# Kernel optimization log

Hardware: AMD Instinct MI355X
Metric: run time of the kernel (lower is better)

## Reference

```python
import jax, jax.numpy as jnp
import numpy as np

N = 100000      # nodes
E = 1600000     # nonzeros in sparse H (avg degree 16)
IN_DIM = 128
HID = 128
OUT = 128


def setup_inputs() -> dict:
    key = jax.random.key(0)
    k = jax.random.split(key, 8)
    X = jax.random.normal(k[0], (N, IN_DIM), dtype=jnp.float32)
    H_rows = jax.random.randint(k[1], (E,), 0, N, dtype=jnp.int32)
    H_cols = jax.random.randint(k[2], (E,), 0, N, dtype=jnp.int32)
    H_vals = jax.random.uniform(k[3], (E,), dtype=jnp.float32)
    # Linear params (PyTorch: y = x @ W.T + b); store as [in, out] for x @ W
    s1 = 1.0 / np.sqrt(IN_DIM)
    s2 = 1.0 / np.sqrt(HID)
    W1 = jax.random.uniform(k[4], (IN_DIM, HID), jnp.float32, -s1, s1)
    b1 = jax.random.uniform(k[5], (HID,), jnp.float32, -s1, s1)
    W2 = jax.random.uniform(k[6], (HID, OUT), jnp.float32, -s2, s2)
    b2 = jax.random.uniform(k[7], (OUT,), jnp.float32, -s2, s2)
    return {"X": X, "H_rows": H_rows, "H_cols": H_cols, "H_vals": H_vals,
            "W1": W1, "b1": b1, "W2": W2, "b2": b2}


def _spmm(rows, cols, vals, X):
    # sparse [N,N] @ dense [N,d] via edge gather + segment-sum
    msgs = vals[:, None] * X[cols]            # [E, d]
    return jax.ops.segment_sum(msgs, rows, num_segments=N)


def reference(X, H_rows, H_cols, H_vals, W1, b1, W2, b2):
    # num_layers == 2 branch; dropout is identity (eval mode)
    h = _spmm(H_rows, H_cols, H_vals, X @ W1 + b1)   # H @ W1(X)
    h = jax.nn.relu(h)
    out = _spmm(H_rows, H_cols, H_vals, h @ W2 + b2) # H @ W2(h)
    return out
```

## Files before the change

### kernel.cpp

```cpp
#include <hip/hip_runtime.h>

#define NNODES 100000
#define DIM 128
#define BROWS 256
#define NB ((NNODES + BROWS - 1) / BROWS)
#define BCAP 5120
#define CHUNK 4096

__device__ __forceinline__ float f4c(const float4& v, int q) {
    switch (q) { case 0: return v.x; case 1: return v.y; case 2: return v.z; }
    return v.w;
}

__device__ __forceinline__ unsigned int pack_bf16x2(float lo, float hi) {
    unsigned int ul = __float_as_uint(lo);
    unsigned int uh = __float_as_uint(hi);
    ul = (ul + 0x7fffu + ((ul >> 16) & 1u)) >> 16;
    uh = (uh + 0x7fffu + ((uh >> 16) & 1u)) & 0xffff0000u;
    return uh | ul;
}

__device__ __forceinline__ void unpack_bf16x8(uint4 v, float* f) {
    f[0] = __uint_as_float(v.x << 16); f[1] = __uint_as_float(v.x & 0xffff0000u);
    f[2] = __uint_as_float(v.y << 16); f[3] = __uint_as_float(v.y & 0xffff0000u);
    f[4] = __uint_as_float(v.z << 16); f[5] = __uint_as_float(v.z & 0xffff0000u);
    f[6] = __uint_as_float(v.w << 16); f[7] = __uint_as_float(v.w & 0xffff0000u);
}

template <bool IN_BF16>
__global__ __launch_bounds__(256, 2) void gemm_tile(const void* __restrict__ Ain,
                                                    const float* __restrict__ W,
                                                    const float* __restrict__ bias,
                                                    unsigned short* __restrict__ Yb, int n) {
    __shared__ float as[128 * 36];
    __shared__ float bs[32 * 128];
    const int t = threadIdx.x;
    const int tx = t & 15, ty = t >> 4;
    const int row0 = blockIdx.x * 128;
    const int r_lo = ty * 4;
    const int c_lo = tx * 4;

    float acc[8][8];
    {
        const float4 bv0 = *(const float4*)&bias[c_lo];
        const float4 bv1 = *(const float4*)&bias[64 + c_lo];
#pragma unroll
        for (int i = 0; i < 8; ++i) {
            acc[i][0] = bv0.x; acc[i][1] = bv0.y; acc[i][2] = bv0.z; acc[i][3] = bv0.w;
            acc[i][4] = bv1.x; acc[i][5] = bv1.y; acc[i][6] = bv1.z; acc[i][7] = bv1.w;
        }
    }

    const float4* W4 = (const float4*)W;

    for (int kp = 0; kp < 4; ++kp) {
        if (IN_BF16) {
            const uint4* A16 = (const uint4*)Ain;
#pragma unroll
            for (int j = 0; j < 2; ++j) {
                const int l = t + j * 256;
                const int row = l >> 2, ch = l & 3;
                const int rr = row0 + row;
                uint4 v = make_uint4(0u, 0u, 0u, 0u);
                if (rr < n) v = A16[(size_t)rr * 16 + kp * 4 + ch];
                float f[8];
                unpack_bf16x8(v, f);
                float* dst = &as[row * 36 + ch * 8];
                *(float4*)&dst[0] = make_float4(f[0], f[1], f[2], f[3]);
                *(float4*)&dst[4] = make_float4(f[4], f[5], f[6], f[7]);
            }
        } else {
            const float4* A4 = (const float4*)Ain;
#pragma unroll
            for (int j = 0; j < 4; ++j) {
                const int l = t + j * 256;
                const int row = l >> 3, k4 = l & 7;
                const int rr = row0 + row;
                float4 v = make_float4(0.f, 0.f, 0.f, 0.f);
                if (rr < n) v = A4[(size_t)rr * 32 + kp * 8 + k4];
                *(float4*)&as[row * 36 + k4 * 4] = v;
            }
        }
#pragma unroll
        for (int j = 0; j < 4; ++j) {
            const int l = t + j * 256;
            const int k = l >> 5, c4 = l & 31;
            *(float4*)&bs[k * 128 + c4 * 4] = W4[(size_t)(kp * 32 + k) * 32 + c4];
        }
        __syncthreads();

#pragma unroll 2
        for (int kk = 0; kk < 32; kk += 4) {
            float4 a[8], b0[4], b1[4];
#pragma unroll
            for (int i = 0; i < 4; ++i) {
                a[i]     = *(const float4*)&as[(r_lo + i) * 36 + kk];
                a[4 + i] = *(const float4*)&as[(64 + r_lo + i) * 36 + kk];
            }
#pragma unroll
            for (int q = 0; q < 4; ++q) {
                b0[q] = *(const float4*)&bs[(kk + q) * 128 + c_lo];
                b1[q] = *(const float4*)&bs[(kk + q) * 128 + 64 + c_lo];
            }
#pragma unroll
            for (int q = 0; q < 4; ++q) {
#pragma unroll
                for (int i = 0; i < 8; ++i) {
                    const float av = f4c(a[i], q);
                    acc[i][0] = fmaf(av, b0[q].x, acc[i][0]);
                    acc[i][1] = fmaf(av, b0[q].y, acc[i][1]);
                    acc[i][2] = fmaf(av, b0[q].z, acc[i][2]);
                    acc[i][3] = fmaf(av, b0[q].w, acc[i][3]);
                    acc[i][4] = fmaf(av, b1[q].x, acc[i][4]);
                    acc[i][5] = fmaf(av, b1[q].y, acc[i][5]);
                    acc[i][6] = fmaf(av, b1[q].z, acc[i][6]);
                    acc[i][7] = fmaf(av, b1[q].w, acc[i][7]);
                }
            }
        }
        __syncthreads();
    }

#pragma unroll
    for (int i = 0; i < 8; ++i) {
        const int lr = (i < 4) ? (r_lo + i) : (64 + r_lo + i - 4);
        const int rr = row0 + lr;
        if (rr < n) {
            uint2 lo = make_uint2(pack_bf16x2(acc[i][0], acc[i][1]),
                                  pack_bf16x2(acc[i][2], acc[i][3]));
            uint2 hi = make_uint2(pack_bf16x2(acc[i][4], acc[i][5]),
                                  pack_bf16x2(acc[i][6], acc[i][7]));
            *(uint2*)&Yb[(size_t)rr * DIM + c_lo] = lo;
            *(uint2*)&Yb[(size_t)rr * DIM + 64 + c_lo] = hi;
        }
    }
}

__global__ __launch_bounds__(256) void pass1_bin(const int* __restrict__ rows,
                                                 const int* __restrict__ cols,
                                                 const float* __restrict__ vals,
                                                 int* __restrict__ bcnt,
                                                 int2* __restrict__ tmp, int nnz) {
    __shared__ int hist[NB];
    __shared__ int base[NB];
    __shared__ int cur[NB];
    const int t = threadIdx.x;
    const int e0 = blockIdx.x * CHUNK;
    const int e1 = min(e0 + CHUNK, nnz);

    for (int i = t; i < NB; i += 256) { hist[i] = 0; cur[i] = 0; }
    __syncthreads();

    for (int i = e0 + t; i < e1; i += 256)
        atomicAdd(&hist[rows[i] >> 8], 1);
    __syncthreads();

    for (int i = t; i < NB; i += 256)
        base[i] = (hist[i] > 0) ? atomicAdd(&bcnt[i], hist[i]) : 0;
    __syncthreads();

    for (int i = e0 + t; i < e1; i += 256) {
        const int r = rows[i];
        const int b = r >> 8;
        const int pos = base[b] + atomicAdd(&cur[b], 1);
        if (pos < BCAP)
            tmp[(size_t)b * BCAP + pos] =
                make_int2(((r & 255) << 24) | cols[i], __float_as_int(vals[i]));
    }
}

__global__ __launch_bounds__(512) void scan_buckets(const int* __restrict__ bcnt,
                                                    int* __restrict__ bbase, int nb) {
    __shared__ int s[512];
    const int t = threadIdx.x;
    const int v = (t < nb) ? bcnt[t] : 0;
    s[t] = v;
    __syncthreads();
    for (int off = 1; off < 512; off <<= 1) {
        int x = (t >= off) ? s[t - off] : 0;
        __syncthreads();
        s[t] += x;
        __syncthreads();
    }
    if (t < nb) bbase[t] = s[t] - v;
}

__global__ __launch_bounds__(256) void pass2_sort(const int2* __restrict__ tmp,
                                                  const int* __restrict__ bcnt,
                                                  const int* __restrict__ bbase,
                                                  int2* __restrict__ epack,
                                                  int* __restrict__ row_ptr,
                                                  int* __restrict__ counts, int n) {
    __shared__ int cnt[256];
    __shared__ int s[256];
    __shared__ int cur[256];
    const int b = blockIdx.x;
    const int t = threadIdx.x;
    const int row0 = b * BROWS;
    const int nrows = min(BROWS, n - row0);
    const int m = min(bcnt[b], BCAP);
    const int base = bbase[b];
    const int2* __restrict__ src = tmp + (size_t)b * BCAP;

    cnt[t] = 0;
    __syncthreads();
    for (int i = t; i < m; i += 256)
        atomicAdd(&cnt[((unsigned)src[i].x) >> 24], 1);
    __syncthreads();

    const int v = cnt[t];
    s[t] = v;
    __syncthreads();
    for (int off = 1; off < 256; off <<= 1) {
        int x = (t >= off) ? s[t - off] : 0;
        __syncthreads();
        s[t] += x;
        __syncthreads();
    }
    const int excl = s[t] - v;
    if (t < nrows) {
        row_ptr[row0 + t] = base + excl;
        counts[row0 + t] = v;
    }
    cur[t] = base + excl;
    __syncthreads();

    for (int i = t; i < m; i += 256) {
        const int2 e = src[i];
        const int rl = ((unsigned)e.x) >> 24;
        const int pos = atomicAdd(&cur[rl], 1);
        epack[pos] = make_int2(e.x & 0xFFFFFF, e.y);
    }
}

template <bool RELU_OUT, bool OUT_BF16>
__global__ __launch_bounds__(256) void spmm_csr(const int* __restrict__ row_ptr,
                                                const int* __restrict__ counts,
                                                const int2* __restrict__ epack,
                                                const unsigned short* __restrict__ Xb,
                                                void* __restrict__ out, int n) {
    const int gid = blockIdx.x * blockDim.x + threadIdx.x;
    const int r = gid >> 4;
    const int lane = gid & 15;
    if (r >= n) return;
    const int start = row_ptr[r];
    const int cnt = counts[r];
    const uint4* __restrict__ X16 = (const uint4*)Xb;
    const int2* __restrict__ ep = epack + start;

    float acc[8];
#pragma unroll
    for (int k = 0; k < 8; ++k) acc[k] = 0.f;

    int j = 0;
    for (; j + 4 <= cnt; j += 4) {
        const int2 e0 = ep[j], e1 = ep[j + 1], e2 = ep[j + 2], e3 = ep[j + 3];
        const uint4 x0 = X16[(size_t)e0.x * 16 + lane];
        const uint4 x1 = X16[(size_t)e1.x * 16 + lane];
        const uint4 x2 = X16[(size_t)e2.x * 16 + lane];
        const uint4 x3 = X16[(size_t)e3.x * 16 + lane];
        const float v0 = __int_as_float(e0.y), v1 = __int_as_float(e1.y);
        const float v2 = __int_as_float(e2.y), v3 = __int_as_float(e3.y);
        float f0[8], f1[8], f2[8], f3[8];
        unpack_bf16x8(x0, f0); unpack_bf16x8(x1, f1);
        unpack_bf16x8(x2, f2); unpack_bf16x8(x3, f3);
#pragma unroll
        for (int k = 0; k < 8; ++k)
            acc[k] += v0 * f0[k] + v1 * f1[k] + v2 * f2[k] + v3 * f3[k];
    }
    for (; j < cnt; ++j) {
        const int2 e = ep[j];
        const uint4 x = X16[(size_t)e.x * 16 + lane];
        const float v = __int_as_float(e.y);
        float f[8];
        unpack_bf16x8(x, f);
#pragma unroll
        for (int k = 0; k < 8; ++k) acc[k] += v * f[k];
    }

    if (RELU_OUT) {
#pragma unroll
        for (int k = 0; k < 8; ++k) acc[k] = fmaxf(acc[k], 0.f);
    }

    if (OUT_BF16) {
        uint4 pv = make_uint4(pack_bf16x2(acc[0], acc[1]), pack_bf16x2(acc[2], acc[3]),
                              pack_bf16x2(acc[4], acc[5]), pack_bf16x2(acc[6], acc[7]));
        ((uint4*)out)[(size_t)r * 16 + lane] = pv;
    } else {
        float* of = (float*)out;
        *(float4*)&of[(size_t)r * DIM + lane * 8]     = make_float4(acc[0], acc[1], acc[2], acc[3]);
        *(float4*)&of[(size_t)r * DIM + lane * 8 + 4] = make_float4(acc[4], acc[5], acc[6], acc[7]);
    }
}

extern "C" void kernel_launch(void* const* d_in, const int* in_sizes, int n_in,
                              void* d_out, int out_size, void* d_ws, size_t ws_size,
                              hipStream_t stream) {
    const float* X      = (const float*)d_in[0];
    const int*   H_rows = (const int*)d_in[1];
    const int*   H_cols = (const int*)d_in[2];
    const float* H_vals = (const float*)d_in[3];
    const float* W1     = (const float*)d_in[4];
    const float* b1     = (const float*)d_in[5];
    const float* W2     = (const float*)d_in[6];
    const float* b2     = (const float*)d_in[7];
    float* out = (float*)d_out;

    const int E = in_sizes[1];
    const int N = NNODES;
    const size_t bmat_bytes = (size_t)N * DIM * 2;

    const int gemm_blocks = (N + 127) / 128;
    const int p1_blocks = (E + CHUNK - 1) / CHUNK;
    const int spmm_blocks = (N * 16 + 255) / 256;

    char* p = (char*)d_ws;
    unsigned short* Yb = (unsigned short*)p;  p += bmat_bytes;
    unsigned short* hb = (unsigned short*)p;  p += bmat_bytes;
    int2* epack        = (int2*)p;            p += (size_t)E * 8;
    int2* tmp          = (int2*)p;            p += (size_t)NB * BCAP * 8;
    int*  bcnt         = (int*)p;             p += (size_t)NB * 4;
    int*  bbase        = (int*)p;             p += (size_t)NB * 4;
    int*  row_ptr      = (int*)p;             p += (size_t)N * 4;
    int*  counts       = (int*)p;             p += (size_t)N * 4;

    hipMemsetAsync(bcnt, 0, (size_t)NB * 4, stream);
    pass1_bin<<<p1_blocks, 256, 0, stream>>>(H_rows, H_cols, H_vals, bcnt, tmp, E);
    scan_buckets<<<1, 512, 0, stream>>>(bcnt, bbase, NB);
    pass2_sort<<<NB, 256, 0, stream>>>(tmp, bcnt, bbase, epack, row_ptr, counts, N);

    gemm_tile<false><<<gemm_blocks, 256, 0, stream>>>(X, W1, b1, Yb, N);
    spmm_csr<true, true><<<spmm_blocks, 256, 0, stream>>>(row_ptr, counts, epack, Yb, hb, N);

    gemm_tile<true><<<gemm_blocks, 256, 0, stream>>>(hb, W2, b2, Yb, N);
    spmm_csr<false, false><<<spmm_blocks, 256, 0, stream>>>(row_ptr, counts, epack, Yb, out, N);
}
```

Baseline: 397.6 us.

## Replace FP32 SIMT GEMM with FP16 MFMA GEMM using pre-transposed weights

Swaps the shared-memory tiled FP32 FMA GEMM for a register-only kernel built on 16x16x32 f16 MFMA instructions. Each wave loads its 32 input rows straight from global memory into half8 fragments. A new prep kernel transposes and converts W1/W2 to FP16 so weight fragments load contiguously. This targets the dense-layer compute cost but lowers input and weight precision to FP16. Weight fragments are also reloaded from global memory per block rather than staged in LDS.

Result: faster. 364.1 us (-8.4%).

```diff
diff --git a/kernel.cpp b/kernel.cpp
--- a/kernel.cpp
+++ b/kernel.cpp
@@ -7,10 +7,8 @@
 #define BCAP 5120
 #define CHUNK 4096
 
-__device__ __forceinline__ float f4c(const float4& v, int q) {
-    switch (q) { case 0: return v.x; case 1: return v.y; case 2: return v.z; }
-    return v.w;
-}
+typedef _Float16 half8 __attribute__((ext_vector_type(8)));
+typedef float f32x4 __attribute__((ext_vector_type(4)));
 
 __device__ __forceinline__ unsigned int pack_bf16x2(float lo, float hi) {
     unsigned int ul = __float_as_uint(lo);
@@ -27,111 +25,104 @@
     f[6] = __uint_as_float(v.w << 16); f[7] = __uint_as_float(v.w & 0xffff0000u);
 }
 
+__global__ __launch_bounds__(256) void prep_w(const float* __restrict__ W1s,
+                                              const float* __restrict__ W2s,
+                                              _Float16* __restrict__ Wt1,
+                                              _Float16* __restrict__ Wt2) {
+    const int b = blockIdx.x;
+    const float* __restrict__ W = (b & 4) ? W2s : W1s;
+    _Float16* __restrict__ Wt = (b & 4) ? Wt2 : Wt1;
+    const int base = (b & 3) * 4096;
+    for (int i = threadIdx.x; i < 4096; i += 256) {
+        const int e = base + i;
+        const int k = e >> 7, c = e & 127;
+        Wt[c * 128 + k] = (_Float16)W[e];
+    }
+}
+
 template <bool IN_BF16>
-__global__ __launch_bounds__(256, 2) void gemm_tile(const void* __restrict__ Ain,
-                                                    const float* __restrict__ W,
-                                                    const float* __restrict__ bias,
-                                                    unsigned short* __restrict__ Yb, int n) {
-    __shared__ float as[128 * 36];
-    __shared__ float bs[32 * 128];
+__global__ __launch_bounds__(256) void gemm_mfma(const void* __restrict__ Ain,
+                                                 const _Float16* __restrict__ Wt,
+                                                 const float* __restrict__ bias,
+                                                 unsigned short* __restrict__ Yb, int n) {
     const int t = threadIdx.x;
-    const int tx = t & 15, ty = t >> 4;
-    const int row0 = blockIdx.x * 128;
-    const int r_lo = ty * 4;
-    const int c_lo = tx * 4;
-
-    float acc[8][8];
-    {
-        const float4 bv0 = *(const float4*)&bias[c_lo];
-        const float4 bv1 = *(const float4*)&bias[64 + c_lo];
-#pragma unroll
-        for (int i = 0; i < 8; ++i) {
-            acc[i][0] = bv0.x; acc[i][1] = bv0.y; acc[i][2] = bv0.z; acc[i][3] = bv0.w;
-            acc[i][4] = bv1.x; acc[i][5] = bv1.y; acc[i][6] = bv1.z; acc[i][7] = bv1.w;
-        }
-    }
-
-    const float4* W4 = (const float4*)W;
-
-    for (int kp = 0; kp < 4; ++kp) {
+    const int l = t & 63;
+    const int lr = l & 15;
+    const int lg = l >> 4;
+    const int r0 = blockIdx.x * 128 + (t >> 6) * 32;
+
+    half8 xf[2][4];
+#pragma unroll
+    for (int rt = 0; rt < 2; ++rt) {
+        const int row = r0 + rt * 16 + lr;
+        const bool ok = row < n;
         if (IN_BF16) {
-            const uint4* A16 = (const uint4*)Ain;
-#pragma unroll
-            for (int j = 0; j < 2; ++j) {
-                const int l = t + j * 256;
-                const int row = l >> 2, ch = l & 3;
-                const int rr = row0 + row;
+            const uint4* __restrict__ A16 = (const uint4*)Ain;
+#pragma unroll
+            for (int ks = 0; ks < 4; ++ks) {
                 uint4 v = make_uint4(0u, 0u, 0u, 0u);
-                if (rr < n) v = A16[(size_t)rr * 16 + kp * 4 + ch];
+                if (ok) v = A16[(size_t)row * 16 + ks * 4 + lg];
                 float f[8];
                 unpack_bf16x8(v, f);
-                float* dst = &as[row * 36 + ch * 8];
-                *(float4*)&dst[0] = make_float4(f[0], f[1], f[2], f[3]);
-                *(float4*)&dst[4] = make_float4(f[4], f[5], f[6], f[7]);
+                half8 h;
+#pragma unroll
+                for (int j = 0; j < 8; ++j) h[j] = (_Float16)f[j];
+                xf[rt][ks] = h;
             }
         } else {
-            const float4* A4 = (const float4*)Ain;
-#pragma unroll
-            for (int j = 0; j < 4; ++j) {
-                const int l = t + j * 256;
-                const int row = l >> 3, k4 = l & 7;
-                const int rr = row0 + row;
-                float4 v = make_float4(0.f, 0.f, 0.f, 0.f);
-                if (rr < n) v = A4[(size_t)rr * 32 + kp * 8 + k4];
-                *(float4*)&as[row * 36 + k4 * 4] = v;
+            const float4* __restrict__ A4 = (const float4*)Ain;
+#pragma unroll
+            for (int ks = 0; ks < 4; ++ks) {
+                float4 v0 = make_float4(0.f, 0.f, 0.f, 0.f);
+                float4 v1 = v0;
+                if (ok) {
+                    v0 = A4[(size_t)row * 32 + ks * 8 + lg * 2];
+                    v1 = A4[(size_t)row * 32 + ks * 8 + lg * 2 + 1];
+                }
+                half8 h;
+                h[0] = (_Float16)v0.x; h[1] = (_Float16)v0.y;
+                h[2] = (_Float16)v0.z; h[3] = (_Float16)v0.w;
+                h[4] = (_Float16)v1.x; h[5] = (_Float16)v1.y;
+                h[6] = (_Float16)v1.z; h[7] = (_Float16)v1.w;
+                xf[rt][ks] = h;
             }
         }
-#pragma unroll
-        for (int j = 0; j < 4; ++j) {
-            const int l = t + j * 256;
-            const int k = l >> 5, c4 = l & 31;
-            *(float4*)&bs[k * 128 + c4 * 4] = W4[(size_t)(kp * 32 + k) * 32 + c4];
+    }
+
+    const f32x4 zero4 = {0.f, 0.f, 0.f, 0.f};
+    f32x4 acc[2][8];
+#pragma unroll
+    for (int rt = 0; rt < 2; ++rt)
+#pragma unroll
+        for (int ct = 0; ct < 8; ++ct) acc[rt][ct] = zero4;
+
+    const half8* __restrict__ Wf = (const half8*)Wt;
+#pragma unroll
+    for (int ct = 0; ct < 8; ++ct) {
+        half8 wf[4];
+#pragma unroll
+        for (int ks = 0; ks < 4; ++ks)
+            wf[ks] = Wf[(ct * 16 + lr) * 16 + ks * 4 + lg];
+#pragma unroll
+        for (int ks = 0; ks < 4; ++ks) {
+            acc[0][ct] = __builtin_amdgcn_mfma_f32_16x16x32_f16(wf[ks], xf[0][ks], acc[0][ct], 0, 0, 0);
+            acc[1][ct] = __builtin_amdgcn_mfma_f32_16x16x32_f16(wf[ks], xf[1][ks], acc[1][ct], 0, 0, 0);
         }
-        __syncthreads();
-
-#pragma unroll 2
-        for (int kk = 0; kk < 32; kk += 4) {
-            float4 a[8], b0[4], b1[4];
-#pragma unroll
-            for (int i = 0; i < 4; ++i) {
-                a[i]     = *(const float4*)&as[(r_lo + i) * 36 + kk];
-                a[4 + i] = *(const float4*)&as[(64 + r_lo + i) * 36 + kk];
+    }
+
+#pragma unroll
+    for (int ct = 0; ct < 8; ++ct) {
+        const int c0 = ct * 16 + lg * 4;
+        const float4 bv = *(const float4*)&bias[c0];
+#pragma unroll
+        for (int rt = 0; rt < 2; ++rt) {
+            const int row = r0 + rt * 16 + lr;
+            if (row < n) {
+                f32x4 a = acc[rt][ct];
+                uint2 pv = make_uint2(pack_bf16x2(a[0] + bv.x, a[1] + bv.y),
+                                      pack_bf16x2(a[2] + bv.z, a[3] + bv.w));
+                *(uint2*)&Yb[(size_t)row * DIM + c0] = pv;
             }
-#pragma unroll
-            for (int q = 0; q < 4; ++q) {
-                b0[q] = *(const float4*)&bs[(kk + q) * 128 + c_lo];
-                b1[q] = *(const float4*)&bs[(kk + q) * 128 + 64 + c_lo];
-            }
-#pragma unroll
-            for (int q = 0; q < 4; ++q) {
-#pragma unroll
-                for (int i = 0; i < 8; ++i) {
-                    const float av = f4c(a[i], q);
-                    acc[i][0] = fmaf(av, b0[q].x, acc[i][0]);
-                    acc[i][1] = fmaf(av, b0[q].y, acc[i][1]);
-                    acc[i][2] = fmaf(av, b0[q].z, acc[i][2]);
-                    acc[i][3] = fmaf(av, b0[q].w, acc[i][3]);
-                    acc[i][4] = fmaf(av, b1[q].x, acc[i][4]);
-                    acc[i][5] = fmaf(av, b1[q].y, acc[i][5]);
-                    acc[i][6] = fmaf(av, b1[q].z, acc[i][6]);
-                    acc[i][7] = fmaf(av, b1[q].w, acc[i][7]);
-                }
-            }
-        }
-        __syncthreads();
-    }
-
-#pragma unroll
-    for (int i = 0; i < 8; ++i) {
-        const int lr = (i < 4) ? (r_lo + i) : (64 + r_lo + i - 4);
-        const int rr = row0 + lr;
-        if (rr < n) {
-            uint2 lo = make_uint2(pack_bf16x2(acc[i][0], acc[i][1]),
-                                  pack_bf16x2(acc[i][2], acc[i][3]));
-            uint2 hi = make_uint2(pack_bf16x2(acc[i][4], acc[i][5]),
-                                  pack_bf16x2(acc[i][6], acc[i][7]));
-            *(uint2*)&Yb[(size_t)rr * DIM + c_lo] = lo;
-            *(uint2*)&Yb[(size_t)rr * DIM + 64 + c_lo] = hi;
         }
     }
 }
@@ -318,6 +309,8 @@
     char* p = (char*)d_ws;
     unsigned short* Yb = (unsigned short*)p;  p += bmat_bytes;
     unsigned short* hb = (unsigned short*)p;  p += bmat_bytes;
+    _Float16* Wt1      = (_Float16*)p;        p += 128 * 128 * 2;
+    _Float16* Wt2      = (_Float16*)p;        p += 128 * 128 * 2;
     int2* epack        = (int2*)p;            p += (size_t)E * 8;
     int2* tmp          = (int2*)p;            p += (size_t)NB * BCAP * 8;
     int*  bcnt         = (int*)p;             p += (size_t)NB * 4;
@@ -325,14 +318,16 @@
     int*  row_ptr      = (int*)p;             p += (size_t)N * 4;
     int*  counts       = (int*)p;             p += (size_t)N * 4;
 
+    prep_w<<<8, 256, 0, stream>>>(W1, W2, Wt1, Wt2);
+
     hipMemsetAsync(bcnt, 0, (size_t)NB * 4, stream);
     pass1_bin<<<p1_blocks, 256, 0, stream>>>(H_rows, H_cols, H_vals, bcnt, tmp, E);
     scan_buckets<<<1, 512, 0, stream>>>(bcnt, bbase, NB);
     pass2_sort<<<NB, 256, 0, stream>>>(tmp, bcnt, bbase, epack, row_ptr, counts, N);
 
-    gemm_tile<false><<<gemm_blocks, 256, 0, stream>>>(X, W1, b1, Yb, N);
+    gemm_mfma<false><<<gemm_blocks, 256, 0, stream>>>(X, Wt1, b1, Yb, N);
     spmm_csr<true, true><<<spmm_blocks, 256, 0, stream>>>(row_ptr, counts, epack, Yb, hb, N);
 
-    gemm_tile<true><<<gemm_blocks, 256, 0, stream>>>(hb, W2, b2, Yb, N);
+    gemm_mfma<true><<<gemm_blocks, 256, 0, stream>>>(hb, Wt2, b2, Yb, N);
     spmm_csr<false, false><<<spmm_blocks, 256, 0, stream>>>(row_ptr, counts, epack, Yb, out, N);
 }
```
